# Performance work log

Hardware: AMD Instinct MI355X
Metric: run time of the kernel (lower is better)

The kernel has to match this reference:

```python
import jax, jax.numpy as jnp
import numpy as np

B, S, D, H, M, V, R = 2, 1024, 768, 8, 3072, 32000, 2
HD = D // H  # head_dim = qkv_dim // num_heads


def ln(x, scale, bias, eps=1e-6):
    m = jnp.mean(x, axis=-1, keepdims=True)
    v = jnp.mean(jnp.square(x - m), axis=-1, keepdims=True)
    return (x - m) * jax.lax.rsqrt(v + eps) * scale + bias


def setup_inputs() -> dict:
    key = jax.random.key(0)
    ks = jax.random.split(key, 16)
    r = lambda i, shp, s=0.02: jax.random.normal(ks[i], shp, jnp.float32) * s
    z = lambda shp: jnp.zeros(shp, jnp.float32)
    o = lambda shp: jnp.ones(shp, jnp.float32)
    return {
        'l2r_embed': jax.random.normal(ks[0], (B, S, D), jnp.float32),
        'r2l_embed': jax.random.normal(ks[1], (B, S, D), jnp.float32),
        'temb': jax.random.normal(ks[2], (B, D), jnp.float32),
        'ln_l2r_s': o((D,)), 'ln_l2r_b': z((D,)),
        'ln_r2l_s': o((D,)), 'ln_r2l_b': z((D,)),
        'Wq': r(3, (D, H, HD)), 'bq': z((H, HD)),
        'Wk': r(4, (D, H, HD)), 'bk': z((H, HD)),
        'Wv': r(5, (D, H, HD)), 'bv': z((H, HD)),
        'Wo': r(6, (H, HD, D)), 'bo': z((D,)),
        'ff_ln_s': o((D,)), 'ff_ln_b': z((D,)),
        'ff_w1': r(7, (D, M)), 'ff_b1': z((M,)),
        'ff_w2': r(8, (M, D)), 'ff_b2': z((D,)),
        'tm_w1': r(9, (D, M)), 'tm_b1': z((M,)),
        'tm_w2': r(10, (M, 4 * D)), 'tm_b2': z((4 * D,)),
        'film_w': r(11, (R, 4 * D, 2 * D)), 'film_b': z((R, 2 * D)),
        'r_w1': r(12, (R, D, M)), 'r_b1': z((R, M)),
        'r_w2': r(13, (R, M, D)), 'r_b2': z((R, D)),
        'r_ln_s': o((R, D)), 'r_ln_b': z((R, D)),
        'out_w': r(14, (D, V)), 'out_b': z((V,)),
    }


def reference(l2r_embed, r2l_embed, temb, ln_l2r_s, ln_l2r_b, ln_r2l_s, ln_r2l_b,
              Wq, bq, Wk, bk, Wv, bv, Wo, bo, ff_ln_s, ff_ln_b,
              ff_w1, ff_b1, ff_w2, ff_b2, tm_w1, tm_b1, tm_w2, tm_b2,
              film_w, film_b, r_w1, r_b1, r_w2, r_b2, r_ln_s, r_ln_b,
              out_w, out_b):
    inputs = l2r_embed + r2l_embed
    # prenorm on each direction (temb stays raw)
    l2r_n = ln(l2r_embed, ln_l2r_s, ln_l2r_b)
    r2l_n = ln(r2l_embed, ln_r2l_s, ln_r2l_b)
    # cross attention: query from sum, keys/vals from [temb, l2r, r2l]
    q = jnp.einsum('bsd,dhk->bshk', l2r_n + r2l_n, Wq) + bq
    all_e = jnp.concatenate([temb[:, None, :], l2r_n, r2l_n], axis=1)  # [B, 2S+1, D]
    k = jnp.einsum('bsd,dhk->bshk', all_e, Wk) + bk
    v = jnp.einsum('bsd,dhk->bshk', all_e, Wv) + bv
    q = q / jnp.sqrt(jnp.float32(HD))
    logits = jnp.einsum('bqhd,bkhd->bhqk', q, k)  # [B, H, S, 2S+1]
    idx = jnp.arange(S)
    l2r_mask = idx[:, None] >= idx[None, :]
    r2l_mask = idx[:, None] <= idx[None, :]
    joint = jnp.concatenate(
        [jnp.ones((S, 1), bool), l2r_mask, r2l_mask], axis=-1)[None, None]
    aw = jax.nn.softmax(
        jnp.where(joint, logits, jnp.finfo(jnp.float32).min), axis=-1)
    x = jnp.einsum('bhqk,bkhd->bqhd', aw, v)
    x = jnp.einsum('bqhd,hde->bqe', x, Wo) + bo
    x = x + inputs
    # prenorm FF block
    z = ln(x, ff_ln_s, ff_ln_b)
    z = jax.nn.relu(z @ ff_w1 + ff_b1) @ ff_w2 + ff_b2
    x = x + z
    # residual readout with FiLM conditioning
    t = jax.nn.gelu(temb @ tm_w1 + tm_b1) @ tm_w2 + tm_b2  # [B, 4D]
    for i in range(R):
        film = t @ film_w[i] + film_b[i]  # [B, 2D]
        z = jax.nn.gelu(x @ r_w1[i] + r_b1[i]) @ r_w2[i] + r_b2[i]
        x = ln(x + z, r_ln_s[i], r_ln_b[i])
        a, b = jnp.split(film[:, None, :], 2, axis=-1)
        x = a * x + b
    return x @ out_w + out_b  # [B, S, V]
```

## Files before the change

kernel.cpp:

```cpp
#include <hip/hip_runtime.h>
#include <cstdint>
#include <cstddef>

#define Bb 2
#define Ss 1024
#define Dd 768
#define Hh 8
#define HDh 96
#define Mm 3072
#define Vv 32000
#define KVr 2049

typedef __attribute__((ext_vector_type(8))) short short8v;
typedef __attribute__((ext_vector_type(4))) short short4v;
typedef __attribute__((ext_vector_type(4))) float f32x4;

#define GL16(gp, lp) __builtin_amdgcn_global_load_lds( \
    (const __attribute__((address_space(1))) void*)(gp), \
    (__attribute__((address_space(3))) void*)(lp), 16, 0, 0)

static __device__ __forceinline__ short f2bf(float f) {
  union { float f; unsigned u; } x; x.f = f;
  unsigned r = (x.u + 0x7FFFu + ((x.u >> 16) & 1u)) >> 16;
  return (short)(r & 0xFFFFu);
}

static __device__ __forceinline__ float gelu_f(float v) {
  float u = 0.7978845608028654f * (v + 0.044715f * v * v * v);
  float au = fabsf(u);
  float e = __expf(2.f * au);
  float t = 1.f - 2.f / (e + 1.f);
  return 0.5f * v * (1.f + copysignf(t, u));
}

static __device__ __forceinline__ float blk_sum(float val, float* sh) {
  #pragma unroll
  for (int off = 32; off >= 1; off >>= 1) val += __shfl_xor(val, off);
  __syncthreads();
  if ((threadIdx.x & 63) == 0) sh[threadIdx.x >> 6] = val;
  __syncthreads();
  return sh[0] + sh[1] + sh[2] + sh[3];
}

__global__ __launch_bounds__(256) void prep_kernel(
    const float* __restrict__ l2r, const float* __restrict__ r2l,
    const float* __restrict__ temb,
    const float* __restrict__ s1, const float* __restrict__ b1,
    const float* __restrict__ s2, const float* __restrict__ b2,
    float* __restrict__ inputs, short* __restrict__ qin, short* __restrict__ all_e)
{
  __shared__ float sh[4];
  const int tid = threadIdx.x;
  if (blockIdx.x >= 2048) {
    int b = blockIdx.x - 2048;
    #pragma unroll
    for (int i = 0; i < 3; ++i)
      all_e[(size_t)b * KVr * Dd + tid + i * 256] = f2bf(temb[(size_t)b * Dd + tid + i * 256]);
    return;
  }
  const int row = blockIdx.x;
  const int b = row >> 10, s = row & 1023;
  const float* ap = l2r + (size_t)row * Dd;
  const float* cp = r2l + (size_t)row * Dd;
  float a0 = ap[tid], a1 = ap[tid + 256], a2 = ap[tid + 512];
  float c0 = cp[tid], c1 = cp[tid + 256], c2 = cp[tid + 512];
  float ma = blk_sum(a0 + a1 + a2, sh) * (1.f / 768.f);
  float mc = blk_sum(c0 + c1 + c2, sh) * (1.f / 768.f);
  float va = blk_sum((a0-ma)*(a0-ma) + (a1-ma)*(a1-ma) + (a2-ma)*(a2-ma), sh) * (1.f / 768.f);
  float vc = blk_sum((c0-mc)*(c0-mc) + (c1-mc)*(c1-mc) + (c2-mc)*(c2-mc), sh) * (1.f / 768.f);
  float ia = rsqrtf(va + 1e-6f), ic = rsqrtf(vc + 1e-6f);
  size_t ro = (size_t)row * Dd;
  size_t e1 = ((size_t)b * KVr + 1 + s) * Dd;
  size_t e2 = ((size_t)b * KVr + 1 + Ss + s) * Dd;
  float av[3] = {a0, a1, a2}, cv[3] = {c0, c1, c2};
  #pragma unroll
  for (int i = 0; i < 3; ++i) {
    int c = tid + i * 256;
    float an = (av[i] - ma) * ia * s1[c] + b1[c];
    float cn = (cv[i] - mc) * ic * s2[c] + b2[c];
    inputs[ro + c] = av[i] + cv[i];
    qin[ro + c]    = f2bf(an + cn);
    all_e[e1 + c]  = f2bf(an);
    all_e[e2 + c]  = f2bf(cn);
  }
}

__global__ __launch_bounds__(256) void ln_kernel(
    const float* __restrict__ x, const float* __restrict__ sc, const float* __restrict__ bi,
    short* __restrict__ yb)
{
  __shared__ float sh[4];
  const int row = blockIdx.x, tid = threadIdx.x;
  const float* xr = x + (size_t)row * Dd;
  float v0 = xr[tid], v1 = xr[tid + 256], v2 = xr[tid + 512];
  float m = blk_sum(v0 + v1 + v2, sh) * (1.f / 768.f);
  float var = blk_sum((v0-m)*(v0-m) + (v1-m)*(v1-m) + (v2-m)*(v2-m), sh) * (1.f / 768.f);
  float inv = rsqrtf(var + 1e-6f);
  float vv[3] = {v0, v1, v2};
  #pragma unroll
  for (int i = 0; i < 3; ++i) {
    int c = tid + i * 256;
    yb[(size_t)row * Dd + c] = f2bf((vv[i] - m) * inv * sc[c] + bi[c]);
  }
}

__global__ __launch_bounds__(256) void ln_comb(
    const float* __restrict__ pk,
    const float* __restrict__ bias, const float* __restrict__ res,
    const float* __restrict__ sc, const float* __restrict__ bi,
    const float* __restrict__ film, float* __restrict__ yf, short* __restrict__ yb)
{
  __shared__ float sh[4];
  const int row = blockIdx.x, tid = threadIdx.x;
  const size_t PS = (size_t)2048 * 768;
  size_t ro = (size_t)row * Dd;
  float vv[3];
  #pragma unroll
  for (int i = 0; i < 3; ++i) {
    int c = tid + i * 256;
    float v = bias[c] + res[ro + c];
    #pragma unroll
    for (int s = 0; s < 4; ++s) v += pk[s * PS + ro + c];
    vv[i] = v;
  }
  float m = blk_sum(vv[0] + vv[1] + vv[2], sh) * (1.f / 768.f);
  float var = blk_sum((vv[0]-m)*(vv[0]-m) + (vv[1]-m)*(vv[1]-m) + (vv[2]-m)*(vv[2]-m), sh) * (1.f / 768.f);
  float inv = rsqrtf(var + 1e-6f);
  int bb = row >> 10;
  #pragma unroll
  for (int i = 0; i < 3; ++i) {
    int c = tid + i * 256;
    float o = (vv[i] - m) * inv * sc[c] + bi[c];
    o = film[(size_t)bb * 1536 + c] * o + film[(size_t)bb * 1536 + 768 + c];
    if (yf) yf[ro + c] = o;
    if (yb) yb[ro + c] = f2bf(o);
  }
}

__global__ __launch_bounds__(256) void combine_kernel(
    const float* __restrict__ pk,
    const float* __restrict__ bias, const float* __restrict__ res,
    float* __restrict__ yf, short* __restrict__ yb)
{
  const int row = blockIdx.x, tid = threadIdx.x;
  const size_t PS = (size_t)2048 * 768;
  size_t ro = (size_t)row * Dd;
  #pragma unroll
  for (int i = 0; i < 3; ++i) {
    int c = tid + i * 256;
    float v = bias[c] + res[ro + c];
    #pragma unroll
    for (int s = 0; s < 4; ++s) v += pk[s * PS + ro + c];
    yf[ro + c] = v;
    yb[ro + c] = f2bf(v);
  }
}

__global__ __launch_bounds__(256) void convT(const float* __restrict__ W, short* __restrict__ Wt,
                                             int K, int N, int ntile)
{
  __shared__ short T[64][72];
  const int bn = blockIdx.x % ntile, bk = blockIdx.x / ntile;
  const int k0 = bk * 64, n0 = bn * 64, tid = threadIdx.x;
  #pragma unroll
  for (int i = 0; i < 4; ++i) {
    int id = i * 256 + tid;
    int r = id >> 4, c4 = (id & 15) * 4;
    float4 w4 = *(const float4*)(W + (size_t)(k0 + r) * N + n0 + c4);
    T[c4 + 0][r] = f2bf(w4.x);
    T[c4 + 1][r] = f2bf(w4.y);
    T[c4 + 2][r] = f2bf(w4.z);
    T[c4 + 3][r] = f2bf(w4.w);
  }
  __syncthreads();
  #pragma unroll
  for (int i = 0; i < 4; ++i) {
    int id = i * 256 + tid;
    int n = id >> 4, k4 = (id & 15) * 4;
    short4v s = *(const short4v*)&T[n][k4];
    *(short4v*)(Wt + (size_t)(n0 + n) * K + k0 + k4) = s;
  }
}

__global__ __launch_bounds__(256) void convT2(const float* __restrict__ W1, short* __restrict__ D1,
                                              const float* __restrict__ W2, short* __restrict__ D2)
{
  __shared__ short T[64][72];
  const int tid = threadIdx.x;
  const bool second = blockIdx.x >= 576;
  const int id576 = second ? (blockIdx.x - 576) : blockIdx.x;
  const int K = second ? 3072 : 768;
  const int N = second ? 768 : 3072;
  const int ntile = N >> 6;
  const float* W = second ? W2 : W1;
  short* Wt = second ? D2 : D1;
  const int bn = id576 % ntile, bk = id576 / ntile;
  const int k0 = bk * 64, n0 = bn * 64;
  #pragma unroll
  for (int i = 0; i < 4; ++i) {
    int id = i * 256 + tid;
    int r = id >> 4, c4 = (id & 15) * 4;
    float4 w4 = *(const float4*)(W + (size_t)(k0 + r) * N + n0 + c4);
    T[c4 + 0][r] = f2bf(w4.x);
    T[c4 + 1][r] = f2bf(w4.y);
    T[c4 + 2][r] = f2bf(w4.z);
    T[c4 + 3][r] = f2bf(w4.w);
  }
  __syncthreads();
  #pragma unroll
  for (int i = 0; i < 4; ++i) {
    int id = i * 256 + tid;
    int n = id >> 4, k4 = (id & 15) * 4;
    short4v s = *(const short4v*)&T[n][k4];
    *(short4v*)(Wt + (size_t)(n0 + n) * K + k0 + k4) = s;
  }
}

__global__ __launch_bounds__(256) void convT4(const float* __restrict__ W0, const float* __restrict__ W1,
                                              const float* __restrict__ W2, const float* __restrict__ W3,
                                              const float* __restrict__ bk, const float* __restrict__ bv,
                                              short* __restrict__ Wt, float* __restrict__ kvb)
{
  __shared__ short T[64][72];
  const int tid = threadIdx.x;
  if (blockIdx.x == 576) {
    #pragma unroll
    for (int i = 0; i < 6; ++i) {
      int c = i * 256 + tid;
      if (c < 1536) kvb[c] = (c < 768) ? bk[c] : bv[c - 768];
    }
    return;
  }
  const int wsel = blockIdx.x / 144, rem = blockIdx.x % 144;
  const float* W = wsel == 0 ? W0 : wsel == 1 ? W1 : wsel == 2 ? W2 : W3;
  short* dst = Wt + (size_t)wsel * 768 * 768;
  const int bn = rem % 12, bk2 = rem / 12;
  const int k0 = bk2 * 64, n0 = bn * 64;
  #pragma unroll
  for (int i = 0; i < 4; ++i) {
    int id = i * 256 + tid;
    int r = id >> 4, c4 = (id & 15) * 4;
    float4 w4 = *(const float4*)(W + (size_t)(k0 + r) * 768 + n0 + c4);
    T[c4 + 0][r] = f2bf(w4.x);
    T[c4 + 1][r] = f2bf(w4.y);
    T[c4 + 2][r] = f2bf(w4.z);
    T[c4 + 3][r] = f2bf(w4.w);
  }
  __syncthreads();
  #pragma unroll
  for (int i = 0; i < 4; ++i) {
    int id = i * 256 + tid;
    int n = id >> 4, k4 = (id & 15) * 4;
    short4v s = *(const short4v*)&T[n][k4];
    *(short4v*)(dst + (size_t)(n0 + n) * 768 + k0 + k4) = s;
  }
}

template<int ACT>
__global__ __launch_bounds__(256, 4) void gemm_bf(
    const short* __restrict__ A, const short* __restrict__ Bt,
    const float* __restrict__ bias, const float* __restrict__ res,
    float* __restrict__ C, short* __restrict__ Cbf, float* __restrict__ Cpart,
    int M, int N, int K, float scale, int mtiles, int ntiles, int ksplit)
{
  __shared__ short As[2][4096];
  __shared__ short Bs[2][4096];
  const int tid = threadIdx.x, lane = tid & 63, wv = tid >> 6;
  const int l15 = lane & 15, l4 = lane >> 4;

  const int nwg = gridDim.x;
  const int qc = nwg >> 3, rc = nwg & 7;
  const int xcd = blockIdx.x & 7, idx = blockIdx.x >> 3;
  const int wgid = (xcd < rc ? xcd * (qc + 1) : rc * (qc + 1) + (xcd - rc) * qc) + idx;
  const int by = wgid % mtiles;
  const int rest = wgid / mtiles;
  const int bx = rest % ntiles;
  const int sp = rest / ntiles;
  const int kper = K / ksplit;
  const int kbeg = sp * kper;
  const int NT = kper >> 5;

  const int m0 = by * 128, n0 = bx * 128;
  const int wm = (wv >> 1) * 64, wn = (wv & 1) * 64;

  const int srow = lane >> 2, schunk = lane & 3;
  const int scsw = (schunk ^ ((srow >> 1) & 3)) << 3;
  const short* sA = A + (size_t)(m0 + wv * 32 + srow) * K + kbeg + scsw;
  const short* sB = Bt + (size_t)(n0 + wv * 32 + srow) * K + kbeg + scsw;
  const int stBase = wv * 1024;
  const int frsw = (l4 ^ ((l15 >> 1) & 3)) << 3;

  f32x4 acc[4][4];
  const f32x4 zz = {0.f, 0.f, 0.f, 0.f};
  #pragma unroll
  for (int i = 0; i < 4; ++i)
    #pragma unroll
    for (int j = 0; j < 4; ++j) acc[i][j] = zz;

  GL16(sA, &As[0][stBase]);
  GL16(sA + (size_t)16 * K, &As[0][stBase + 512]);
  GL16(sB, &Bs[0][stBase]);
  GL16(sB + (size_t)16 * K, &Bs[0][stBase + 512]);

  int buf = 0;
  for (int t = 0; t < NT; ++t) {
    if (t + 1 < NT) {
      int k0 = (t + 1) << 5;
      GL16(sA + k0, &As[buf ^ 1][stBase]);
      GL16(sA + (size_t)16 * K + k0, &As[buf ^ 1][stBase + 512]);
      GL16(sB + k0, &Bs[buf ^ 1][stBase]);
      GL16(sB + (size_t)16 * K + k0, &Bs[buf ^ 1][stBase + 512]);
      asm volatile("s_waitcnt vmcnt(4)" ::: "memory");
    } else {
      asm volatile("s_waitcnt vmcnt(0)" ::: "memory");
    }
    __builtin_amdgcn_s_barrier();

    short8v af[4], bfv[4];
    #pragma unroll
    for (int mi = 0; mi < 4; ++mi)
      af[mi] = *(const short8v*)&As[buf][(wm + mi * 16 + l15) * 32 + frsw];
    #pragma unroll
    for (int ni = 0; ni < 4; ++ni)
      bfv[ni] = *(const short8v*)&Bs[buf][(wn + ni * 16 + l15) * 32 + frsw];
    __builtin_amdgcn_s_setprio(1);
    #pragma unroll
    for (int mi = 0; mi < 4; ++mi)
      #pragma unroll
      for (int ni = 0; ni < 4; ++ni)
        acc[mi][ni] = __builtin_amdgcn_mfma_f32_16x16x32_bf16(af[mi], bfv[ni], acc[mi][ni], 0, 0, 0);
    __builtin_amdgcn_s_setprio(0);
    if (t + 1 < NT) __builtin_amdgcn_s_barrier();
    buf ^= 1;
  }

  if (Cpart) {
    float* Cp = Cpart + (size_t)sp * M * N;
    #pragma unroll
    for (int mi = 0; mi < 4; ++mi)
      #pragma unroll
      for (int r = 0; r < 4; ++r) {
        int row = m0 + wm + mi * 16 + l4 * 4 + r;
        if (row >= M) continue;
        size_t rb = (size_t)row * N;
        #pragma unroll
        for (int ni = 0; ni < 4; ++ni)
          Cp[rb + n0 + wn + ni * 16 + l15] = acc[mi][ni][r];
      }
    return;
  }

  #pragma unroll
  for (int mi = 0; mi < 4; ++mi) {
    #pragma unroll
    for (int r = 0; r < 4; ++r) {
      int row = m0 + wm + mi * 16 + l4 * 4 + r;
      if (row >= M) continue;
      size_t rb = (size_t)row * N;
      #pragma unroll
      for (int ni = 0; ni < 4; ++ni) {
        int col = n0 + wn + ni * 16 + l15;
        float val = (acc[mi][ni][r] + bias[col]) * scale;
        if (ACT == 1) val = fmaxf(val, 0.f);
        if (ACT == 2) val = gelu_f(val);
        if (res) val += res[rb + col];
        if (C)   C[rb + col] = val;
        if (Cbf) Cbf[rb + col] = f2bf(val);
      }
    }
  }
}

__global__ __launch_bounds__(512, 2) void gemm256(
    const short* __restrict__ A, const short* __restrict__ Bt,
    const float* __restrict__ bias, float* __restrict__ C,
    int M, int N, int K, int mtiles)
{
  __shared__ short As[2][16384];
  __shared__ short Bs[2][16384];
  const int tid = threadIdx.x, lane = tid & 63, wv = tid >> 6;
  const int l15 = lane & 15, l4 = lane >> 4;

  const int nwg = gridDim.x;
  const int qc = nwg >> 3, rc = nwg & 7;
  const int xcd = blockIdx.x & 7, idx = blockIdx.x >> 3;
  const int wgid = (xcd < rc ? xcd * (qc + 1) : rc * (qc + 1) + (xcd - rc) * qc) + idx;
  const int by = wgid % mtiles, bx = wgid / mtiles;
  const int m0 = by * 256, n0 = bx * 256;
  const int wm = (wv >> 2) * 128, wn = (wv & 3) * 64;

  const int srow = lane >> 2, schunk = lane & 3;
  const int scsw = (schunk ^ ((srow >> 1) & 3)) << 3;
  const short* sA = A + (size_t)(m0 + wv * 16 + srow) * K + scsw;
  const short* sB = Bt + (size_t)(n0 + wv * 16 + srow) * K + scsw;
  const int stBase = wv * 512;
  const int frsw = (l4 ^ ((l15 >> 1) & 3)) << 3;

  #define STG_A(b, kk, ko) do { \
    GL16(sA + (ko) + (kk) * 32,                  &As[b][(kk) * 8192 + stBase]); \
    GL16(sA + (size_t)128 * K + (ko) + (kk) * 32, &As[b][(kk) * 8192 + 4096 + stBase]); } while (0)
  #define STG_B(b, kk, ko) do { \
    GL16(sB + (ko) + (kk) * 32,                  &Bs[b][(kk) * 8192 + stBase]); \
    GL16(sB + (size_t)128 * K + (ko) + (kk) * 32, &Bs[b][(kk) * 8192 + 4096 + stBase]); } while (0)
  #define ARD(b, kk, row) (*(const short8v*)&As[b][(kk) * 8192 + (row) * 32 + frsw])
  #define BRD(b, kk, row) (*(const short8v*)&Bs[b][(kk) * 8192 + (row) * 32 + frsw])

  f32x4 acc[8][4];
  const f32x4 zz = {0.f, 0.f, 0.f, 0.f};
  #pragma unroll
  for (int i = 0; i < 8; ++i)
    #pragma unroll
    for (int j = 0; j < 4; ++j) acc[i][j] = zz;

  const int NT = K >> 6;

  STG_A(0, 0, 0); STG_B(0, 0, 0); STG_A(0, 1, 0); STG_B(0, 1, 0);
  asm volatile("s_waitcnt vmcnt(4)" ::: "memory");
  __builtin_amdgcn_s_barrier();

  int buf = 0;
  for (int t = 0; t < NT; ++t) {
    const bool pf = (t + 1 < NT);
    const int k1 = (t + 1) << 6;
    short8v af[4], bfv[4];

    #pragma unroll
    for (int mi = 0; mi < 4; ++mi) af[mi] = ARD(buf, 0, wm + mi * 16 + l15);
    #pragma unroll
    for (int ni = 0; ni < 4; ++ni) bfv[ni] = BRD(buf, 0, wn + ni * 16 + l15);
    if (pf) STG_A(buf ^ 1, 0, k1);
    __builtin_amdgcn_s_barrier();
    asm volatile("s_waitcnt lgkmcnt(0)" ::: "memory");
    __builtin_amdgcn_sched_barrier(0);
    __builtin_amdgcn_s_setprio(1);
    #pragma unroll
    for (int mi = 0; mi < 4; ++mi)
      #pragma unroll
      for (int ni = 0; ni < 4; ++ni)
        acc[mi][ni] = __builtin_amdgcn_mfma_f32_16x16x32_bf16(af[mi], bfv[ni], acc[mi][ni], 0, 0, 0);
    __builtin_amdgcn_s_setprio(0);
    __builtin_amdgcn_s_barrier();

    #pragma unroll
    for (int mi = 0; mi < 4; ++mi) af[mi] = ARD(buf, 0, wm + 64 + mi * 16 + l15);
    if (pf) STG_B(buf ^ 1, 0, k1);
    __builtin_amdgcn_s_barrier();
    asm volatile("s_waitcnt lgkmcnt(0)" ::: "memory");
    __builtin_amdgcn_sched_barrier(0);
    __builtin_amdgcn_s_setprio(1);
    #pragma unroll
    for (int mi = 0; mi < 4; ++mi)
      #pragma unroll
      for (int ni = 0; ni < 4; ++ni)
        acc[4 + mi][ni] = __builtin_amdgcn_mfma_f32_16x16x32_bf16(af[mi], bfv[ni], acc[4 + mi][ni], 0, 0, 0);
    __builtin_amdgcn_s_setprio(0);
    if (pf) asm volatile("s_waitcnt vmcnt(4)" ::: "memory");
    else    asm volatile("s_waitcnt vmcnt(0)" ::: "memory");
    __builtin_amdgcn_s_barrier();

    #pragma unroll
    for (int mi = 0; mi < 4; ++mi) af[mi] = ARD(buf, 1, wm + mi * 16 + l15);
    #pragma unroll
    for (int ni = 0; ni < 4; ++ni) bfv[ni] = BRD(buf, 1, wn + ni * 16 + l15);
    if (pf) STG_A(buf ^ 1, 1, k1);
    __builtin_amdgcn_s_barrier();
    asm volatile("s_waitcnt lgkmcnt(0)" ::: "memory");
    __builtin_amdgcn_sched_barrier(0);
    __builtin_amdgcn_s_setprio(1);
    #pragma unroll
    for (int mi = 0; mi < 4; ++mi)
      #pragma unroll
      for (int ni = 0; ni < 4; ++ni)
        acc[mi][ni] = __builtin_amdgcn_mfma_f32_16x16x32_bf16(af[mi], bfv[ni], acc[mi][ni], 0, 0, 0);
    __builtin_amdgcn_s_setprio(0);
    __builtin_amdgcn_s_barrier();

    #pragma unroll
    for (int mi = 0; mi < 4; ++mi) af[mi] = ARD(buf, 1, wm + 64 + mi * 16 + l15);
    if (pf) STG_B(buf ^ 1, 1, k1);
    __builtin_amdgcn_s_barrier();
    asm volatile("s_waitcnt lgkmcnt(0)" ::: "memory");
    __builtin_amdgcn_sched_barrier(0);
    __builtin_amdgcn_s_setprio(1);
    #pragma unroll
    for (int mi = 0; mi < 4; ++mi)
      #pragma unroll
      for (int ni = 0; ni < 4; ++ni)
        acc[4 + mi][ni] = __builtin_amdgcn_mfma_f32_16x16x32_bf16(af[mi], bfv[ni], acc[4 + mi][ni], 0, 0, 0);
    __builtin_amdgcn_s_setprio(0);
    if (pf) asm volatile("s_waitcnt vmcnt(4)" ::: "memory");
    __builtin_amdgcn_s_barrier();

    buf ^= 1;
  }

  #pragma unroll
  for (int mi = 0; mi < 8; ++mi) {
    #pragma unroll
    for (int r = 0; r < 4; ++r) {
      int row = m0 + wm + mi * 16 + l4 * 4 + r;
      size_t rb = (size_t)row * N;
      #pragma unroll
      for (int ni = 0; ni < 4; ++ni) {
        int col = n0 + wn + ni * 16 + l15;
        C[rb + col] = acc[mi][ni][r] + bias[col];
      }
    }
  }
  #undef STG_A
  #undef STG_B
  #undef ARD
  #undef BRD
}

__global__ __launch_bounds__(256) void attn_kernel(
    const short* __restrict__ q, const short* __restrict__ kv, short* __restrict__ o)
{
  __shared__ short Kls[64][104];
  __shared__ short Vt[96][72];
  __shared__ short Pls[4][16][72];

  const int tid = threadIdx.x, lane = tid & 63, w = tid >> 6;
  const int l15 = lane & 15, l4 = lane >> 4;
  const int qt = blockIdx.x & 15;
  const int bh = blockIdx.x >> 4;
  const int h = bh & 7, b = bh >> 3;
  const int qb = qt * 64;
  const int qw = qb + w * 16;

  short8v qf[3];
  {
    const short* qp = q + ((size_t)(b * Ss + qw + l15)) * Dd + h * HDh + l4 * 8;
    #pragma unroll
    for (int kk = 0; kk < 3; ++kk) qf[kk] = *(const short8v*)(qp + kk * 32);
  }

  const f32x4 zz = {0.f, 0.f, 0.f, 0.f};
  f32x4 Oa[6];
  #pragma unroll
  for (int fn = 0; fn < 6; ++fn) Oa[fn] = zz;
  float mrow[4], lrow[4];
  #pragma unroll
  for (int r = 0; r < 4; ++r) { mrow[r] = -3.0e38f; lrow[r] = 0.f; }

  const size_t kvbase = (size_t)b * KVr;

  for (int t = 0; t < 33; ++t) {
    int k0 = t * 64;
    bool l2r_vis = (k0 <= Ss) && (k0 - 1 <= qb + 63);
    int rmaxk = (k0 + 63 > 2 * Ss) ? 2 * Ss : (k0 + 63);
    bool r2l_vis = (k0 + 63 >= Ss + 1) && (rmaxk - (Ss + 1) >= qb);
    if (!(t == 0 || l2r_vis || r2l_vis)) continue;

    __syncthreads();
    #pragma unroll
    for (int i = 0; i < 3; ++i) {
      int id = i * 256 + tid;
      int row = id / 12, cc = (id % 12) * 8;
      const short* kp = kv + (kvbase + k0 + row) * 1536 + h * HDh + cc;
      short8v k8 = *(const short8v*)kp;
      *(short8v*)&Kls[row][cc] = k8;
      short8v v8 = *(const short8v*)(kp + 768);
      #pragma unroll
      for (int j = 0; j < 8; ++j) Vt[cc + j][row] = v8[j];
    }
    __syncthreads();

    f32x4 sc[4];
    #pragma unroll
    for (int nt = 0; nt < 4; ++nt) {
      f32x4 d = zz;
      #pragma unroll
      for (int kk = 0; kk < 3; ++kk) {
        short8v kf = *(const short8v*)&Kls[nt * 16 + l15][kk * 32 + l4 * 8];
        d = __builtin_amdgcn_mfma_f32_16x16x32_bf16(qf[kk], kf, d, 0, 0, 0);
      }
      sc[nt] = d;
    }
    float tmax[4] = {-3.0e38f, -3.0e38f, -3.0e38f, -3.0e38f};
    #pragma unroll
    for (int nt = 0; nt < 4; ++nt)
      #pragma unroll
      for (int r = 0; r < 4; ++r) {
        int qg = qw + l4 * 4 + r;
        int j = k0 + nt * 16 + l15;
        bool vis = (j == 0) ||
                   (j >= 1 && j <= Ss && (j - 1) <= qg) ||
                   (j >= Ss + 1 && j <= 2 * Ss && (j - (Ss + 1)) >= qg);
        if (!vis) sc[nt][r] = -3.0e38f;
        tmax[r] = fmaxf(tmax[r], sc[nt][r]);
      }
    #pragma unroll
    for (int r = 0; r < 4; ++r) {
      #pragma unroll
      for (int off = 8; off >= 1; off >>= 1) tmax[r] = fmaxf(tmax[r], __shfl_xor(tmax[r], off));
    }
    float scl[4];
    #pragma unroll
    for (int r = 0; r < 4; ++r) {
      float mnew = fmaxf(mrow[r], tmax[r]);
      scl[r] = __expf(mrow[r] - mnew);
      mrow[r] = mnew;
    }
    #pragma unroll
    for (int fn = 0; fn < 6; ++fn)
      #pragma unroll
      for (int r = 0; r < 4; ++r) Oa[fn][r] *= scl[r];
    float lad[4] = {0.f, 0.f, 0.f, 0.f};
    #pragma unroll
    for (int nt = 0; nt < 4; ++nt)
      #pragma unroll
      for (int r = 0; r < 4; ++r) {
        float p = __expf(sc[nt][r] - mrow[r]);
        lad[r] += p;
        Pls[w][l4 * 4 + r][nt * 16 + l15] = f2bf(p);
      }
    #pragma unroll
    for (int r = 0; r < 4; ++r) {
      #pragma unroll
      for (int off = 8; off >= 1; off >>= 1) lad[r] += __shfl_xor(lad[r], off);
      lrow[r] = lrow[r] * scl[r] + lad[r];
    }
    __syncthreads();

    short8v pf[2];
    #pragma unroll
    for (int kk = 0; kk < 2; ++kk) pf[kk] = *(const short8v*)&Pls[w][l15][kk * 32 + l4 * 8];
    #pragma unroll
    for (int fn = 0; fn < 6; ++fn) {
      #pragma unroll
      for (int kk = 0; kk < 2; ++kk) {
        short8v vf = *(const short8v*)&Vt[fn * 16 + l15][kk * 32 + l4 * 8];
        Oa[fn] = __builtin_amdgcn_mfma_f32_16x16x32_bf16(pf[kk], vf, Oa[fn], 0, 0, 0);
      }
    }
  }

  #pragma unroll
  for (int fn = 0; fn < 6; ++fn)
    #pragma unroll
    for (int r = 0; r < 4; ++r) {
      int row = qw + l4 * 4 + r;
      int col = h * HDh + fn * 16 + l15;
      o[((size_t)(b * Ss + row)) * Dd + col] = f2bf(Oa[fn][r] / lrow[r]);
    }
}

__global__ __launch_bounds__(256) void thin1(const float* __restrict__ A, const float* __restrict__ W,
                                             float* __restrict__ part, int K, int N, int nblk, int splits)
{
  __shared__ float a0s[64], a1s[64];
  const int nb = blockIdx.x % nblk, ks = blockIdx.x / nblk;
  const int kl = K / splits, kbeg = ks * kl;
  const int tid = threadIdx.x;
  for (int k = tid; k < kl; k += 256) { a0s[k] = A[kbeg + k]; a1s[k] = A[K + kbeg + k]; }
  __syncthreads();
  const int n = nb * 256 + tid;
  float acc0 = 0.f, acc1 = 0.f;
  for (int k = 0; k < kl; ++k) {
    float w = W[(size_t)(kbeg + k) * N + n];
    acc0 = fmaf(a0s[k], w, acc0);
    acc1 = fmaf(a1s[k], w, acc1);
  }
  part[(size_t)ks * 2 * N + n] = acc0;
  part[(size_t)ks * 2 * N + N + n] = acc1;
}

__global__ __launch_bounds__(256) void thin1p(
    const float* __restrict__ pin, const float* __restrict__ bin,
    const float* __restrict__ W, float* __restrict__ part)
{
  __shared__ float a0s[48], a1s[48];
  const int nb = blockIdx.x % 12, ks = blockIdx.x / 12;
  const int kbeg = ks * 48, tid = threadIdx.x;
  for (int j = tid; j < 96; j += 256) {
    int row = j / 48, k = j % 48;
    float v = bin[kbeg + k];
    for (int s = 0; s < 64; ++s) v += pin[(size_t)s * 6144 + (size_t)row * 3072 + kbeg + k];
    v = gelu_f(v);
    if (row) a1s[k] = v; else a0s[k] = v;
  }
  __syncthreads();
  const int n = nb * 256 + tid;
  float acc0 = 0.f, acc1 = 0.f;
  for (int k = 0; k < 48; ++k) {
    float w = W[(size_t)(kbeg + k) * 3072 + n];
    acc0 = fmaf(a0s[k], w, acc0);
    acc1 = fmaf(a1s[k], w, acc1);
  }
  part[(size_t)ks * 6144 + n] = acc0;
  part[(size_t)ks * 6144 + 3072 + n] = acc1;
}

__global__ __launch_bounds__(256) void film1p(
    const float* __restrict__ pin, const float* __restrict__ bin,
    const float* __restrict__ W, float* __restrict__ part)
{
  __shared__ float a0s[48], a1s[48];
  const int nb = blockIdx.x % 12, ks = blockIdx.x / 12;
  const int kbeg = ks * 48, tid = threadIdx.x;
  for (int j = tid; j < 96; j += 256) {
    int row = j / 48, k = j % 48;
    float v = bin[kbeg + k];
    for (int s = 0; s < 64; ++s) v += pin[(size_t)s * 6144 + (size_t)row * 3072 + kbeg + k];
    if (row) a1s[k] = v; else a0s[k] = v;
  }
  __syncthreads();
  const int n = nb * 256 + tid;
  const int col = (n >= 1536) ? (n - 1536) : n;
  const float* Wp = W + ((n < 1536) ? (size_t)0 : (size_t)3072 * 1536)
                      + (size_t)kbeg * 1536 + col;
  float acc0 = 0.f, acc1 = 0.f;
  for (int k = 0; k < 48; ++k) {
    float w = Wp[(size_t)k * 1536];
    acc0 = fmaf(a0s[k], w, acc0);
    acc1 = fmaf(a1s[k], w, acc1);
  }
  part[(size_t)ks * 6144 + n] = acc0;
  part[(size_t)ks * 6144 + 3072 + n] = acc1;
}

__global__ __launch_bounds__(256) void film2(const float* __restrict__ part,
                                             const float* __restrict__ fb,
                                             float* __restrict__ f0, float* __restrict__ f1)
{
  const int n = blockIdx.x * 256 + threadIdx.x;
  float a0 = fb[n], a1 = a0;
  for (int s = 0; s < 64; ++s) {
    a0 += part[(size_t)s * 6144 + n];
    a1 += part[(size_t)s * 6144 + 3072 + n];
  }
  float* dst = (n < 1536) ? f0 : f1;
  const int c = (n >= 1536) ? (n - 1536) : n;
  dst[c] = a0;
  dst[1536 + c] = a1;
}

static void gemm_launch(int act, const short* A, const short* Bt, const float* bias,
                        const float* res, float* C, short* Cbf, float* Cpart,
                        int M, int N, int K, float scale, int ksplit, hipStream_t s)
{
  int mt = (M + 127) >> 7, nt = N >> 7;
  dim3 grid(mt * nt * ksplit), blk(256);
  if (act == 1)      gemm_bf<1><<<grid, blk, 0, s>>>(A, Bt, bias, res, C, Cbf, Cpart, M, N, K, scale, mt, nt, ksplit);
  else if (act == 2) gemm_bf<2><<<grid, blk, 0, s>>>(A, Bt, bias, res, C, Cbf, Cpart, M, N, K, scale, mt, nt, ksplit);
  else               gemm_bf<0><<<grid, blk, 0, s>>>(A, Bt, bias, res, C, Cbf, Cpart, M, N, K, scale, mt, nt, ksplit);
}

static void conv_launch(const float* W, short* Wt, int K, int N, hipStream_t s)
{
  int nt = N >> 6, kt = K >> 6;
  convT<<<dim3(nt * kt), dim3(256), 0, s>>>(W, Wt, K, N, nt);
}

extern "C" void kernel_launch(void* const* d_in, const int* in_sizes, int n_in,
                              void* d_out, int out_size, void* d_ws, size_t ws_size,
                              hipStream_t stream)
{
  (void)in_sizes; (void)n_in; (void)out_size; (void)ws_size;
  const float* l2r      = (const float*)d_in[0];
  const float* r2l      = (const float*)d_in[1];
  const float* temb     = (const float*)d_in[2];
  const float* ln_l2r_s = (const float*)d_in[3];
  const float* ln_l2r_b = (const float*)d_in[4];
  const float* ln_r2l_s = (const float*)d_in[5];
  const float* ln_r2l_b = (const float*)d_in[6];
  const float* Wq = (const float*)d_in[7];
  const float* bq = (const float*)d_in[8];
  const float* Wk = (const float*)d_in[9];
  const float* bk = (const float*)d_in[10];
  const float* Wv = (const float*)d_in[11];
  const float* bv = (const float*)d_in[12];
  const float* Wo = (const float*)d_in[13];
  const float* bo = (const float*)d_in[14];
  const float* ff_ln_s = (const float*)d_in[15];
  const float* ff_ln_b = (const float*)d_in[16];
  const float* ff_w1 = (const float*)d_in[17];
  const float* ff_b1 = (const float*)d_in[18];
  const float* ff_w2 = (const float*)d_in[19];
  const float* ff_b2 = (const float*)d_in[20];
  const float* tm_w1 = (const float*)d_in[21];
  const float* tm_b1 = (const float*)d_in[22];
  const float* tm_w2 = (const float*)d_in[23];
  const float* tm_b2 = (const float*)d_in[24];
  const float* film_w = (const float*)d_in[25];
  const float* film_b = (const float*)d_in[26];
  const float* r_w1 = (const float*)d_in[27];
  const float* r_b1 = (const float*)d_in[28];
  const float* r_w2 = (const float*)d_in[29];
  const float* r_b2 = (const float*)d_in[30];
  const float* r_ln_s = (const float*)d_in[31];
  const float* r_ln_b = (const float*)d_in[32];
  const float* out_w = (const float*)d_in[33];
  const float* out_b = (const float*)d_in[34];

  uint8_t* base = (uint8_t*)d_ws;
  short* qin_bf  = (short*)(base + 0);
  short* alle_bf = (short*)(base + 3145728);
  short* qb      = (short*)(base + 9440256);
  short* kvbuf   = (short*)(base + 12585984);
  short* attn_bf = (short*)(base + 25175040);
  float* inputs  = (float*)(base + 28320768);
  float* xbuf    = (float*)(base + 34612224);
  short* xn_bf   = (short*)(base + 40903680);
  short* big_bf  = (short*)(base + 44049408);
  float* x2f     = (float*)(base + 56632320);
  short* x2bf    = (short*)(base + 62923776);
  float* x3f     = (float*)(base + 72360960);
  short* x3bf    = (short*)(base + 78652416);
  short* x4bf    = (short*)(base + 81798144);
  short* wslot   = (short*)(base + 84943872);
  uint8_t* sm    = base + 89662464;
  float* f0    = (float*)(sm + 0);
  float* f1    = (float*)(sm + 12288);
  float* kvbia = (float*)(sm + 24576);
  short* w2slot = (short*)inputs;
  float* part2a = (float*)(base + 44049408);
  float* part2b = (float*)(base + 44049408 + 1572864);
  float* part2c = (float*)(base + 44049408 + 3145728);
  float* partK = (float*)(base + 0);
  short* outwT = (short*)(base + 0);

  const float qscale = 0.1020620726159658f;
  dim3 blk(256);

  thin1<<<dim3(12 * 64), blk, 0, stream>>>(temb, tm_w1, part2a, 768, 3072, 12, 64);
  thin1p<<<dim3(12 * 64), blk, 0, stream>>>(part2a, tm_b1, tm_w2, part2b);
  film1p<<<dim3(12 * 64), blk, 0, stream>>>(part2b, tm_b2, film_w, part2c);
  film2<<<dim3(12), blk, 0, stream>>>(part2c, film_b, f0, f1);

  prep_kernel<<<2050, blk, 0, stream>>>(l2r, r2l, temb, ln_l2r_s, ln_l2r_b, ln_r2l_s, ln_r2l_b,
                                        inputs, qin_bf, alle_bf);

  convT4<<<dim3(577), blk, 0, stream>>>(Wq, Wk, Wv, Wo, bk, bv, wslot, kvbia);

  gemm_launch(0, qin_bf, wslot, bq, nullptr, nullptr, qb, nullptr, 2048, 768, 768, qscale, 1, stream);
  gemm_launch(0, alle_bf, wslot + (size_t)768 * 768, kvbia, nullptr, nullptr, kvbuf, nullptr, 4098, 1536, 768, 1.f, 1, stream);

  attn_kernel<<<256, blk, 0, stream>>>(qb, kvbuf, attn_bf);

  gemm_launch(0, attn_bf, wslot + (size_t)3 * 768 * 768, bo, inputs, xbuf, nullptr, nullptr, 2048, 768, 768, 1.f, 1, stream);
  ln_kernel<<<2048, blk, 0, stream>>>(xbuf, ff_ln_s, ff_ln_b, xn_bf);

  convT2<<<dim3(1152), blk, 0, stream>>>(ff_w1, wslot, ff_w2, w2slot);
  gemm_launch(1, xn_bf, wslot, ff_b1, nullptr, nullptr, big_bf, nullptr, 2048, 3072, 768, 1.f, 1, stream);
  gemm_launch(0, big_bf, w2slot, nullptr, nullptr, nullptr, nullptr, partK, 2048, 768, 3072, 1.f, 4, stream);
  combine_kernel<<<2048, blk, 0, stream>>>(partK, ff_b2, xbuf, x2f, x2bf);

  convT2<<<dim3(1152), blk, 0, stream>>>(r_w1, wslot, r_w2, w2slot);
  gemm_launch(2, x2bf, wslot, r_b1, nullptr, nullptr, big_bf, nullptr, 2048, 3072, 768, 1.f, 1, stream);
  gemm_launch(0, big_bf, w2slot, nullptr, nullptr, nullptr, nullptr, partK, 2048, 768, 3072, 1.f, 4, stream);
  ln_comb<<<2048, blk, 0, stream>>>(partK, r_b2, x2f, r_ln_s, r_ln_b, f0, x3f, x3bf);

  convT2<<<dim3(1152), blk, 0, stream>>>(r_w1 + (size_t)768 * 3072, wslot,
                                         r_w2 + (size_t)3072 * 768, w2slot);
  gemm_launch(2, x3bf, wslot, r_b1 + 3072, nullptr, nullptr, big_bf, nullptr, 2048, 3072, 768, 1.f, 1, stream);
  gemm_launch(0, big_bf, w2slot, nullptr, nullptr, nullptr, nullptr, partK, 2048, 768, 3072, 1.f, 4, stream);
  ln_comb<<<2048, blk, 0, stream>>>(partK, r_b2 + 768, x3f, r_ln_s + 768, r_ln_b + 768, f1, nullptr, x4bf);

  conv_launch(out_w, outwT, 768, 32000, stream);
  gemm256<<<dim3(8 * 125), dim3(512), 0, stream>>>(x4bf, outwT, out_b, (float*)d_out,
                                                   2048, 32000, 768, 8);
}
```

Baseline: 600.1 us.

## Split attention KV loop across two blocks, split-K small GEMMs, fold film2 into convT4

Attention now runs 512 blocks, each handling alternating KV tiles. Each block writes unnormalized fp32 partial outputs plus per-row max and sum, and a new merge kernel combines them flash-decoding style. The Q projection and Wo projection GEMMs switch to split-K=2, with combine kernels that apply bias and scale, or residual plus layernorm. The film reduction kernel is folded into extra blocks of the weight conversion kernel. The aim is to fill more CUs on these small launches, at the cost of extra fp32 partial traffic and extra merge kernels.

Result: faster. 542.2 us (-9.6%).

```diff
diff --git a/kernel.cpp b/kernel.cpp
--- a/kernel.cpp
+++ b/kernel.cpp
@@ -85,22 +85,44 @@
   }
 }
 
-__global__ __launch_bounds__(256) void ln_kernel(
-    const float* __restrict__ x, const float* __restrict__ sc, const float* __restrict__ bi,
-    short* __restrict__ yb)
+__global__ __launch_bounds__(256) void ln_comb2(
+    const float* __restrict__ pk,
+    const float* __restrict__ bias, const float* __restrict__ res,
+    const float* __restrict__ sc, const float* __restrict__ bi,
+    float* __restrict__ yf, short* __restrict__ yb)
 {
   __shared__ float sh[4];
   const int row = blockIdx.x, tid = threadIdx.x;
-  const float* xr = x + (size_t)row * Dd;
-  float v0 = xr[tid], v1 = xr[tid + 256], v2 = xr[tid + 512];
-  float m = blk_sum(v0 + v1 + v2, sh) * (1.f / 768.f);
-  float var = blk_sum((v0-m)*(v0-m) + (v1-m)*(v1-m) + (v2-m)*(v2-m), sh) * (1.f / 768.f);
-  float inv = rsqrtf(var + 1e-6f);
-  float vv[3] = {v0, v1, v2};
+  const size_t PS = (size_t)2048 * 768;
+  size_t ro = (size_t)row * Dd;
+  float vv[3];
   #pragma unroll
   for (int i = 0; i < 3; ++i) {
     int c = tid + i * 256;
-    yb[(size_t)row * Dd + c] = f2bf((vv[i] - m) * inv * sc[c] + bi[c]);
+    vv[i] = pk[ro + c] + pk[PS + ro + c] + bias[c] + res[ro + c];
+  }
+  float m = blk_sum(vv[0] + vv[1] + vv[2], sh) * (1.f / 768.f);
+  float var = blk_sum((vv[0]-m)*(vv[0]-m) + (vv[1]-m)*(vv[1]-m) + (vv[2]-m)*(vv[2]-m), sh) * (1.f / 768.f);
+  float inv = rsqrtf(var + 1e-6f);
+  #pragma unroll
+  for (int i = 0; i < 3; ++i) {
+    int c = tid + i * 256;
+    yf[ro + c] = vv[i];
+    yb[ro + c] = f2bf((vv[i] - m) * inv * sc[c] + bi[c]);
+  }
+}
+
+__global__ __launch_bounds__(256) void scale_comb(
+    const float* __restrict__ pk, const float* __restrict__ bias,
+    short* __restrict__ yb, float scale)
+{
+  const int row = blockIdx.x, tid = threadIdx.x;
+  const size_t PS = (size_t)2048 * 768;
+  size_t ro = (size_t)row * Dd;
+  #pragma unroll
+  for (int i = 0; i < 3; ++i) {
+    int c = tid + i * 256;
+    yb[ro + c] = f2bf((pk[ro + c] + pk[PS + ro + c] + bias[c]) * scale);
   }
 }
 
@@ -219,10 +241,25 @@
 __global__ __launch_bounds__(256) void convT4(const float* __restrict__ W0, const float* __restrict__ W1,
                                               const float* __restrict__ W2, const float* __restrict__ W3,
                                               const float* __restrict__ bk, const float* __restrict__ bv,
-                                              short* __restrict__ Wt, float* __restrict__ kvb)
+                                              short* __restrict__ Wt, float* __restrict__ kvb,
+                                              const float* __restrict__ part2c, const float* __restrict__ fb,
+                                              float* __restrict__ f0, float* __restrict__ f1)
 {
   __shared__ short T[64][72];
   const int tid = threadIdx.x;
+  if (blockIdx.x >= 577) {
+    const int n = (blockIdx.x - 577) * 256 + tid;
+    float a0 = fb[n], a1 = a0;
+    for (int s = 0; s < 64; ++s) {
+      a0 += part2c[(size_t)s * 6144 + n];
+      a1 += part2c[(size_t)s * 6144 + 3072 + n];
+    }
+    float* dst = (n < 1536) ? f0 : f1;
+    const int c = (n >= 1536) ? (n - 1536) : n;
+    dst[c] = a0;
+    dst[1536 + c] = a1;
+    return;
+  }
   if (blockIdx.x == 576) {
     #pragma unroll
     for (int i = 0; i < 6; ++i) {
@@ -514,7 +551,8 @@
 }
 
 __global__ __launch_bounds__(256) void attn_kernel(
-    const short* __restrict__ q, const short* __restrict__ kv, short* __restrict__ o)
+    const short* __restrict__ q, const short* __restrict__ kv,
+    float* __restrict__ Op0, float* __restrict__ Op1, float* __restrict__ ml)
 {
   __shared__ short Kls[64][104];
   __shared__ short Vt[96][72];
@@ -522,8 +560,10 @@
 
   const int tid = threadIdx.x, lane = tid & 63, w = tid >> 6;
   const int l15 = lane & 15, l4 = lane >> 4;
-  const int qt = blockIdx.x & 15;
-  const int bh = blockIdx.x >> 4;
+  const int chunk = blockIdx.x >> 8;
+  const int inner = blockIdx.x & 255;
+  const int qt = inner & 15;
+  const int bh = inner >> 4;
   const int h = bh & 7, b = bh >> 3;
   const int qb = qt * 64;
   const int qw = qb + w * 16;
@@ -545,7 +585,7 @@
 
   const size_t kvbase = (size_t)b * KVr;
 
-  for (int t = 0; t < 33; ++t) {
+  for (int t = chunk; t < 33; t += 2) {
     int k0 = t * 64;
     bool l2r_vis = (k0 <= Ss) && (k0 - 1 <= qb + 63);
     int rmaxk = (k0 + 63 > 2 * Ss) ? 2 * Ss : (k0 + 63);
@@ -636,14 +676,45 @@
     }
   }
 
+  float* Op = chunk ? Op1 : Op0;
   #pragma unroll
   for (int fn = 0; fn < 6; ++fn)
     #pragma unroll
     for (int r = 0; r < 4; ++r) {
       int row = qw + l4 * 4 + r;
       int col = h * HDh + fn * 16 + l15;
-      o[((size_t)(b * Ss + row)) * Dd + col] = f2bf(Oa[fn][r] / lrow[r]);
-    }
+      Op[((size_t)(b * Ss + row)) * Dd + col] = Oa[fn][r];
+    }
+  if (l15 == 0) {
+    #pragma unroll
+    for (int r = 0; r < 4; ++r) {
+      int row = qw + l4 * 4 + r;
+      size_t ix = ((size_t)((chunk * 2 + b) * 8 + h) * 1024 + row) * 2;
+      ml[ix] = mrow[r];
+      ml[ix + 1] = lrow[r];
+    }
+  }
+}
+
+__global__ __launch_bounds__(256) void attn_merge(
+    const float* __restrict__ Op0, const float* __restrict__ Op1,
+    const float* __restrict__ ml, short* __restrict__ o)
+{
+  const int row = blockIdx.x, tid = threadIdx.x;
+  const int b = row >> 10, s = row & 1023;
+  size_t ro = (size_t)row * Dd;
+  #pragma unroll
+  for (int i = 0; i < 3; ++i) {
+    int c = tid + i * 256;
+    int h = c / HDh;
+    size_t ix = ((size_t)(b * 8 + h) * 1024 + s) * 2;
+    float m0 = ml[ix],         l0 = ml[ix + 1];
+    float m1 = ml[32768 + ix], l1 = ml[32768 + ix + 1];
+    float mm = fmaxf(m0, m1);
+    float s0 = __expf(m0 - mm), s1 = __expf(m1 - mm);
+    float denom = s0 * l0 + s1 * l1;
+    o[ro + c] = f2bf((s0 * Op0[ro + c] + s1 * Op1[ro + c]) / denom);
+  }
 }
 
 __global__ __launch_bounds__(256) void thin1(const float* __restrict__ A, const float* __restrict__ W,
@@ -718,22 +789,6 @@
   }
   part[(size_t)ks * 6144 + n] = acc0;
   part[(size_t)ks * 6144 + 3072 + n] = acc1;
-}
-
-__global__ __launch_bounds__(256) void film2(const float* __restrict__ part,
-                                             const float* __restrict__ fb,
-                                             float* __restrict__ f0, float* __restrict__ f1)
-{
-  const int n = blockIdx.x * 256 + threadIdx.x;
-  float a0 = fb[n], a1 = a0;
-  for (int s = 0; s < 64; ++s) {
-    a0 += part[(size_t)s * 6144 + n];
-    a1 += part[(size_t)s * 6144 + 3072 + n];
-  }
-  float* dst = (n < 1536) ? f0 : f1;
-  const int c = (n >= 1536) ? (n - 1536) : n;
-  dst[c] = a0;
-  dst[1536 + c] = a1;
 }
 
 static void gemm_launch(int act, const short* A, const short* Bt, const float* bias,
@@ -818,6 +873,11 @@
   float* part2a = (float*)(base + 44049408);
   float* part2b = (float*)(base + 44049408 + 1572864);
   float* part2c = (float*)(base + 44049408 + 3145728);
+  float* qpart = (float*)(base + 56632320);
+  float* Op0 = (float*)(base + 0);
+  float* mlb = (float*)(base + 6291456);
+  float* Op1 = xbuf;
+  float* wopart = (float*)(base + 0);
   float* partK = (float*)(base + 0);
   short* outwT = (short*)(base + 0);
 
@@ -827,20 +887,22 @@
   thin1<<<dim3(12 * 64), blk, 0, stream>>>(temb, tm_w1, part2a, 768, 3072, 12, 64);
   thin1p<<<dim3(12 * 64), blk, 0, stream>>>(part2a, tm_b1, tm_w2, part2b);
   film1p<<<dim3(12 * 64), blk, 0, stream>>>(part2b, tm_b2, film_w, part2c);
-  film2<<<dim3(12), blk, 0, stream>>>(part2c, film_b, f0, f1);
 
   prep_kernel<<<2050, blk, 0, stream>>>(l2r, r2l, temb, ln_l2r_s, ln_l2r_b, ln_r2l_s, ln_r2l_b,
                                         inputs, qin_bf, alle_bf);
 
-  convT4<<<dim3(577), blk, 0, stream>>>(Wq, Wk, Wv, Wo, bk, bv, wslot, kvbia);
-
-  gemm_launch(0, qin_bf, wslot, bq, nullptr, nullptr, qb, nullptr, 2048, 768, 768, qscale, 1, stream);
+  convT4<<<dim3(589), blk, 0, stream>>>(Wq, Wk, Wv, Wo, bk, bv, wslot, kvbia,
+                                        part2c, film_b, f0, f1);
+
+  gemm_launch(0, qin_bf, wslot, bq, nullptr, nullptr, nullptr, qpart, 2048, 768, 768, 1.f, 2, stream);
+  scale_comb<<<2048, blk, 0, stream>>>(qpart, bq, qb, qscale);
   gemm_launch(0, alle_bf, wslot + (size_t)768 * 768, kvbia, nullptr, nullptr, kvbuf, nullptr, 4098, 1536, 768, 1.f, 1, stream);
 
-  attn_kernel<<<256, blk, 0, stream>>>(qb, kvbuf, attn_bf);
-
-  gemm_launch(0, attn_bf, wslot + (size_t)3 * 768 * 768, bo, inputs, xbuf, nullptr, nullptr, 2048, 768, 768, 1.f, 1, stream);
-  ln_kernel<<<2048, blk, 0, stream>>>(xbuf, ff_ln_s, ff_ln_b, xn_bf);
+  attn_kernel<<<512, blk, 0, stream>>>(qb, kvbuf, Op0, Op1, mlb);
+  attn_merge<<<2048, blk, 0, stream>>>(Op0, Op1, mlb, attn_bf);
+
+  gemm_launch(0, attn_bf, wslot + (size_t)3 * 768 * 768, bo, nullptr, nullptr, nullptr, wopart, 2048, 768, 768, 1.f, 2, stream);
+  ln_comb2<<<2048, blk, 0, stream>>>(wopart, bo, inputs, ff_ln_s, ff_ln_b, xbuf, xn_bf);
 
   convT2<<<dim3(1152), blk, 0, stream>>>(ff_w1, wslot, ff_w2, w2slot);
   gemm_launch(1, xn_bf, wslot, ff_b1, nullptr, nullptr, big_bf, nullptr, 2048, 3072, 768, 1.f, 1, stream);
```
